# Performance work log

Measured on AMD Instinct MI355X. Metric: run time of the kernel, lower is better.

The kernel has to match this reference:

```python
import jax, jax.numpy as jnp
import numpy as np

N = 50000
E = 800000
G = 8
IN, HID, OUT = 128, 256, 128
BN_EPS = 1e-5


def _linear_params(key, fan_in, fan_out):
    k1, k2 = jax.random.split(key)
    s = 1.0 / np.sqrt(fan_in)
    w = jax.random.uniform(k1, (fan_out, fan_in), jnp.float32, -s, s)
    b = jax.random.uniform(k2, (fan_out,), jnp.float32, -s, s)
    return w, b


def setup_inputs() -> dict:
    key = jax.random.key(0)
    ks = jax.random.split(key, 16)
    inp = {
        "x": jax.random.normal(ks[0], (N, IN), jnp.float32),
        "src": jax.random.randint(ks[1], (E,), 0, N, jnp.int32),
        "dst": jax.random.randint(ks[2], (E,), 0, N, jnp.int32),
        "graph_ids": jnp.sort(jax.random.randint(ks[3], (N,), 0, G, jnp.int32)),
    }
    dims = [(IN, HID, HID), (HID, HID, HID), (HID, OUT, OUT)]
    for i, (d_in, d_mid, d_out) in enumerate(dims):
        kk = jax.random.split(ks[4 + i], 2)
        w1, b1 = _linear_params(kk[0], d_in, d_mid)
        w2, b2 = _linear_params(kk[1], d_mid, d_out)
        inp[f"w1_{i}"] = w1
        inp[f"b1_{i}"] = b1
        inp[f"w2_{i}"] = w2
        inp[f"b2_{i}"] = b2
        inp[f"eps_{i}"] = jnp.zeros((), jnp.float32)          # learn_eps, init 0
        inp[f"gamma_{i}"] = jnp.ones((d_out,), jnp.float32)   # BatchNorm weight
        inp[f"beta_{i}"] = jnp.zeros((d_out,), jnp.float32)   # BatchNorm bias
    return inp


def _gin_layer(h, src, dst, w1, b1, w2, b2, eps, gamma, beta):
    # GINConv: (1 + eps) * h_v + sum_{u in N(v)} h_u   (copy_u / sum)
    agg = jax.ops.segment_sum(h[src], dst, num_segments=N)
    z = (1.0 + eps) * h + agg
    # 2-layer MLP with ReLU
    z = jnp.maximum(z @ w1.T + b1, 0.0) @ w2.T + b2
    # BatchNorm1d (training-mode batch statistics, biased variance)
    mu = jnp.mean(z, axis=0)
    var = jnp.var(z, axis=0)
    return (z - mu) * jax.lax.rsqrt(var + BN_EPS) * gamma + beta


def reference(x, src, dst, graph_ids,
              w1_0, b1_0, w2_0, b2_0, eps_0, gamma_0, beta_0,
              w1_1, b1_1, w2_1, b2_1, eps_1, gamma_1, beta_1,
              w1_2, b1_2, w2_2, b2_2, eps_2, gamma_2, beta_2):
    h = _gin_layer(x, src, dst, w1_0, b1_0, w2_0, b2_0, eps_0, gamma_0, beta_0)
    h = jnp.maximum(h, 0.0)  # relu (dropout = identity in eval)
    h = _gin_layer(h, src, dst, w1_1, b1_1, w2_1, b2_1, eps_1, gamma_1, beta_1)
    h = jnp.maximum(h, 0.0)
    h = _gin_layer(h, src, dst, w1_2, b1_2, w2_2, b2_2, eps_2, gamma_2, beta_2)
    # dgl.mean_nodes: per-graph mean over nodes -> [G, OUT]
    sums = jax.ops.segment_sum(h, graph_ids, num_segments=G)
    counts = jax.ops.segment_sum(jnp.ones((N,), h.dtype), graph_ids, num_segments=G)
    return sums / jnp.maximum(counts, 1.0)[:, None]
```

## Files before the change

### kernel.cpp

```cpp
#include <hip/hip_runtime.h>

#define NG 8

typedef _Float16 half8  __attribute__((ext_vector_type(8)));
typedef float    f32x16 __attribute__((ext_vector_type(16)));


__global__ __launch_bounds__(256)
void k_cast16(const float* __restrict__ in, _Float16* __restrict__ out, int n8) {
    int i = blockIdx.x * 256 + threadIdx.x;
    if (i < n8) {
        const float4 a = *(const float4*)(in + (size_t)i * 8);
        const float4 b = *(const float4*)(in + (size_t)i * 8 + 4);
        half8 o;
        o[0] = (_Float16)a.x; o[1] = (_Float16)a.y; o[2] = (_Float16)a.z; o[3] = (_Float16)a.w;
        o[4] = (_Float16)b.x; o[5] = (_Float16)b.y; o[6] = (_Float16)b.z; o[7] = (_Float16)b.w;
        *(half8*)(out + (size_t)i * 8) = o;
    }
}

__global__ __launch_bounds__(256)
void k_castw(const float* __restrict__ w0, const float* __restrict__ w1,
             const float* __restrict__ w2, const float* __restrict__ w3,
             const float* __restrict__ w4, const float* __restrict__ w5,
             _Float16* __restrict__ o0, _Float16* __restrict__ o1,
             _Float16* __restrict__ o2, _Float16* __restrict__ o3,
             _Float16* __restrict__ o4, _Float16* __restrict__ o5) {
    int i = blockIdx.x * 256 + threadIdx.x;
    const float* in; _Float16* out; int off, lgC, K;
    if      (i <  4096) { in = w0; out = o0; off = 0;     lgC = 8; K = 128; }
    else if (i < 12288) { in = w1; out = o1; off = 4096;  lgC = 8; K = 256; }
    else if (i < 20480) { in = w2; out = o2; off = 12288; lgC = 8; K = 256; }
    else if (i < 28672) { in = w3; out = o3; off = 20480; lgC = 8; K = 256; }
    else if (i < 32768) { in = w4; out = o4; off = 28672; lgC = 7; K = 256; }
    else if (i < 34816) { in = w5; out = o5; off = 32768; lgC = 7; K = 128; }
    else return;
    int j = i - off;
    int kslot = j >> lgC;
    int c = j & ((1 << lgC) - 1);
    const float* s = in + (size_t)c * K + kslot * 8;
    const float4 a = *(const float4*)(s);
    const float4 b = *(const float4*)(s + 4);
    half8 o;
    o[0] = (_Float16)a.x; o[1] = (_Float16)a.y; o[2] = (_Float16)a.z; o[3] = (_Float16)a.w;
    o[4] = (_Float16)b.x; o[5] = (_Float16)b.y; o[6] = (_Float16)b.z; o[7] = (_Float16)b.w;
    *(half8*)(out + (size_t)j * 8) = o;
}


__global__ __launch_bounds__(256)
void k_deg(const int* __restrict__ dst, int* __restrict__ deg, int E) {
    int i = blockIdx.x * 256 + threadIdx.x;
    if (i < E) atomicAdd(&deg[dst[i]], 1);
}

__global__ __launch_bounds__(1024)
void k_scan_a(const int* __restrict__ deg, int* __restrict__ incl,
              int* __restrict__ bsum, int n) {
    __shared__ int s[1024];
    int t = threadIdx.x;
    int base = blockIdx.x * 1024;
    int v = (base + t < n) ? deg[base + t] : 0;
    s[t] = v;
    __syncthreads();
    for (int off = 1; off < 1024; off <<= 1) {
        int x = 0;
        if (t >= off) x = s[t - off];
        __syncthreads();
        if (t >= off) s[t] += x;
        __syncthreads();
    }
    if (base + t < n) incl[base + t] = s[t];
    if (t == 1023) bsum[blockIdx.x] = s[1023];
}

__global__ void k_scan_b(int* bsum, int nb) {
    if (threadIdx.x == 0 && blockIdx.x == 0) {
        int run = 0;
        for (int i = 0; i < nb; ++i) { int v = bsum[i]; bsum[i] = run; run += v; }
    }
}

__global__ __launch_bounds__(256)
void k_scan_c(const int* __restrict__ incl, const int* __restrict__ deg,
              const int* __restrict__ bsum, int* __restrict__ rowp, int n) {
    int i = blockIdx.x * 256 + threadIdx.x;
    if (i < n) rowp[i] = incl[i] - deg[i] + bsum[i >> 10];
}

__global__ __launch_bounds__(256)
void k_scatter(const int* __restrict__ src, const int* __restrict__ dst,
               const int* __restrict__ rowp, int* __restrict__ cur,
               int* __restrict__ ss, int E) {
    int i = blockIdx.x * 256 + threadIdx.x;
    if (i < E) {
        int d = dst[i];
        int pos = rowp[d] + atomicAdd(&cur[d], 1);
        ss[pos] = src[i];
    }
}


template<int K, bool AFFINE>
__global__ __launch_bounds__(256)
void k_agg16(const _Float16* __restrict__ h, const int* __restrict__ rowp,
             const int* __restrict__ deg, const int* __restrict__ ss,
             const float* __restrict__ eps, const float* __restrict__ scp,
             const float* __restrict__ shp, _Float16* __restrict__ z, int n) {
    constexpr int TPN = K / 8;
    constexpr int NPB = 256 / TPN;
    int node = blockIdx.x * NPB + threadIdx.x / TPN;
    int lane = threadIdx.x % TPN;
    if (node >= n) return;
    float e1 = 1.0f + eps[0];
    const int c0 = lane * 8;
    float sc[8], sh[8];
    if (AFFINE) {
#pragma unroll
        for (int e = 0; e < 8; ++e) { sc[e] = scp[c0 + e]; sh[e] = shp[c0 + e]; }
    }
    size_t base = (size_t)node * K + c0;
    half8 v = *(const half8*)(h + base);
    float a[8];
#pragma unroll
    for (int e = 0; e < 8; ++e) {
        float f = (float)v[e];
        if (AFFINE) f = fmaxf(f * sc[e] + sh[e], 0.0f);
        a[e] = f * e1;
    }
    int s  = rowp[node];
    int dn = deg[node];
    int j = 0;
    for (; j + 4 <= dn; j += 4) {
        int u0 = ss[s + j], u1 = ss[s + j + 1], u2 = ss[s + j + 2], u3 = ss[s + j + 3];
        half8 h0 = *(const half8*)(h + (size_t)u0 * K + c0);
        half8 h1 = *(const half8*)(h + (size_t)u1 * K + c0);
        half8 h2 = *(const half8*)(h + (size_t)u2 * K + c0);
        half8 h3 = *(const half8*)(h + (size_t)u3 * K + c0);
#pragma unroll
        for (int e = 0; e < 8; ++e) {
            float f0 = (float)h0[e], f1 = (float)h1[e];
            float f2 = (float)h2[e], f3 = (float)h3[e];
            if (AFFINE) {
                f0 = fmaxf(f0 * sc[e] + sh[e], 0.0f);
                f1 = fmaxf(f1 * sc[e] + sh[e], 0.0f);
                f2 = fmaxf(f2 * sc[e] + sh[e], 0.0f);
                f3 = fmaxf(f3 * sc[e] + sh[e], 0.0f);
            }
            a[e] += (f0 + f1) + (f2 + f3);
        }
    }
    for (; j < dn; ++j) {
        int u = ss[s + j];
        half8 hv = *(const half8*)(h + (size_t)u * K + c0);
#pragma unroll
        for (int e = 0; e < 8; ++e) {
            float f = (float)hv[e];
            if (AFFINE) f = fmaxf(f * sc[e] + sh[e], 0.0f);
            a[e] += f;
        }
    }
    half8 o;
#pragma unroll
    for (int e = 0; e < 8; ++e) o[e] = (_Float16)a[e];
    *(half8*)(z + base) = o;
}


template<int K, int MID, int MOUT>
__global__ __launch_bounds__(512)
void k_mlp3(const _Float16* __restrict__ A, const _Float16* __restrict__ W1,
            const float* __restrict__ b1, const _Float16* __restrict__ W2,
            const float* __restrict__ b2, _Float16* __restrict__ C,
            float* __restrict__ partial, int n, int ntiles) {
    constexpr int NK1 = K / 16;
    constexpr int NK2 = MID / 16;
    constexpr int MF1 = (MID == 256) ? 2 : 1;
    constexpr int MF2 = (MOUT == 256) ? 2 : 1;
    constexpr int NLD = K / 64;
    __shared__ char As[64 * 512];
    __shared__ char Ys[64 * 512];
    const int tid  = threadIdx.x;
    const int lane = tid & 63;
    const int wid  = tid >> 6;
    const int lo   = lane & 31;
    const int hi   = lane >> 5;

    const int wc1 = (MID == 256) ? wid : (wid & 3);
    const int wr1 = (MID == 256) ? 0   : (wid >> 2);
    const int colbase1 = wc1 * 32;
    const int wc2 = (MOUT == 256) ? wid : (wid & 3);
    const int wr2 = (MOUT == 256) ? 0   : (wid >> 2);
    const int colbase2 = wc2 * 32;

    half8 w1f[NK1], w2f[NK2];
#pragma unroll
    for (int ks = 0; ks < NK1; ++ks)
        w1f[ks] = *(const half8*)(W1 + ((size_t)(ks * 2 + hi) * MID + colbase1 + lo) * 8);
#pragma unroll
    for (int ks = 0; ks < NK2; ++ks)
        w2f[ks] = *(const half8*)(W2 + ((size_t)(ks * 2 + hi) * MOUT + colbase2 + lo) * 8);
    const float bb1 = b1[colbase1 + lo];
    const float bb2 = b2[colbase2 + lo];

    const int sr = tid >> 3;
    const int sl = tid & 7;
    const int g  = lane & 3;
    const int rl = lane >> 2;
    char* tb = Ys + wid * 2304;

    float s[8], q[8];
#pragma unroll
    for (int e = 0; e < 8; ++e) { s[e] = 0.f; q[e] = 0.f; }

    int tile = blockIdx.x;
    uint4 ar[NLD];
    if (tile < ntiles) {
        int ga = tile * 64 + sr; if (ga > n - 1) ga = n - 1;
        const char* Ab = (const char*)(A + (size_t)ga * K);
#pragma unroll
        for (int i = 0; i < NLD; ++i) ar[i] = *(const uint4*)(Ab + (sl + i * 8) * 16);
    }

    for (; tile < ntiles; tile += gridDim.x) {
        const int brow = tile * 64;

#pragma unroll
        for (int i = 0; i < NLD; ++i)
            *(uint4*)(As + sr * 512 + (((sl + i * 8) ^ (sr & 31)) << 4)) = ar[i];
        int nt = tile + gridDim.x;
        if (nt < ntiles) {
            int ga = nt * 64 + sr; if (ga > n - 1) ga = n - 1;
            const char* Ab = (const char*)(A + (size_t)ga * K);
#pragma unroll
            for (int i = 0; i < NLD; ++i) ar[i] = *(const uint4*)(Ab + (sl + i * 8) * 16);
        }
        __syncthreads();

        f32x16 acc1[MF1];
#pragma unroll
        for (int mf = 0; mf < MF1; ++mf)
#pragma unroll
            for (int e = 0; e < 16; ++e) acc1[mf][e] = 0.0f;
#pragma unroll
        for (int ks = 0; ks < NK1; ++ks) {
#pragma unroll
            for (int mf = 0; mf < MF1; ++mf) {
                int r = ((wr1 + mf) << 5) + lo;
                half8 af = *(const half8*)(As + r * 512 + ((ks * 32 + hi * 16) ^ ((r & 31) << 4)));
                acc1[mf] = __builtin_amdgcn_mfma_f32_32x32x16_f16(af, w1f[ks], acc1[mf], 0, 0, 0);
            }
        }
#pragma unroll
        for (int mf = 0; mf < MF1; ++mf) {
            int rb = ((wr1 + mf) << 5) + (hi << 2);
#pragma unroll
            for (int j = 0; j < 16; ++j) {
                int r = rb + (j & 3) + ((j >> 2) << 3);
                float v = fmaxf(acc1[mf][j] + bb1, 0.0f);
                *(_Float16*)(Ys + r * 512 + (((colbase1 + lo) * 2) ^ ((r & 31) << 4))) = (_Float16)v;
            }
        }
        __syncthreads();

        f32x16 acc2[MF2];
#pragma unroll
        for (int mf = 0; mf < MF2; ++mf)
#pragma unroll
            for (int e = 0; e < 16; ++e) acc2[mf][e] = 0.0f;
#pragma unroll
        for (int ks = 0; ks < NK2; ++ks) {
#pragma unroll
            for (int mf = 0; mf < MF2; ++mf) {
                int r = ((wr2 + mf) << 5) + lo;
                half8 af = *(const half8*)(Ys + r * 512 + ((ks * 32 + hi * 16) ^ ((r & 31) << 4)));
                acc2[mf] = __builtin_amdgcn_mfma_f32_32x32x16_f16(af, w2f[ks], acc2[mf], 0, 0, 0);
            }
        }
        __syncthreads();

#pragma unroll
        for (int mf = 0; mf < MF2; ++mf) {
#pragma unroll
            for (int j = 0; j < 16; ++j) {
                int tr = (j & 3) + ((j >> 2) << 3) + (hi << 2);
                *(_Float16*)(tb + tr * 72 + lo * 2) = (_Float16)(acc2[mf][j] + bb2);
            }
#pragma unroll
            for (int it = 0; it < 2; ++it) {
                int lr = it * 16 + rl;
                int grow = brow + ((wr2 + mf) << 5) + lr;
                half8 v = *(const half8*)(tb + lr * 72 + g * 16);
                if (grow < n) {
                    *(half8*)(C + (size_t)grow * MOUT + colbase2 + g * 8) = v;
#pragma unroll
                    for (int e = 0; e < 8; ++e) { float f = (float)v[e]; s[e] += f; q[e] += f * f; }
                }
            }
        }
    }

#pragma unroll
    for (int e = 0; e < 8; ++e) {
        for (int mk = 4; mk < 64; mk <<= 1) {
            s[e] += __shfl_xor(s[e], mk, 64);
            q[e] += __shfl_xor(q[e], mk, 64);
        }
    }
    if (lane < 4) {
        float* p = partial + ((size_t)blockIdx.x * 2 + wr2) * (2 * MOUT);
#pragma unroll
        for (int e = 0; e < 8; ++e) {
            p[colbase2 + lane * 8 + e]        = s[e];
            p[MOUT + colbase2 + lane * 8 + e] = q[e];
        }
    }
}


template<int M>
__global__ __launch_bounds__(256)
void k_bnred(const float* __restrict__ partial, const float* __restrict__ gamma,
             const float* __restrict__ beta, float* __restrict__ scale,
             float* __restrict__ shift, int n, int count, int step) {
    const int w = threadIdx.x >> 6, lane = threadIdx.x & 63;
    const int c = blockIdx.x * 4 + w;
    float s = 0.f, q = 0.f;
    for (int b = lane; b < count; b += 64) {
        const float* p = partial + (size_t)(b * step) * (2 * M);
        s += p[c];
        q += p[M + c];
    }
#pragma unroll
    for (int mk = 1; mk < 64; mk <<= 1) {
        s += __shfl_xor(s, mk, 64);
        q += __shfl_xor(q, mk, 64);
    }
    if (lane == 0) {
        float invN = 1.0f / (float)n;
        float mean = s * invN;
        float var  = q * invN - mean * mean;
        float sc   = rsqrtf(var + 1e-5f) * gamma[c];
        scale[c] = sc;
        shift[c] = beta[c] - mean * sc;
    }
}


__global__ __launch_bounds__(256)
void k_readout2(const _Float16* __restrict__ z, const float* __restrict__ scale,
                const float* __restrict__ shift, const int* __restrict__ gid,
                float* __restrict__ rpart, int* __restrict__ rcnt, int n) {
    __shared__ float ls[NG * 128];
    __shared__ int   lc[NG];
    for (int i = threadIdx.x; i < NG * 128; i += 256) ls[i] = 0.0f;
    if (threadIdx.x < NG) lc[threadIdx.x] = 0;
    __syncthreads();
    const int c16 = threadIdx.x & 15;
    const int ro  = threadIdx.x >> 4;
    const int c0  = c16 * 8;
    float sc[8], sh[8];
#pragma unroll
    for (int e = 0; e < 8; ++e) { sc[e] = scale[c0 + e]; sh[e] = shift[c0 + e]; }
    for (int r = blockIdx.x * 16 + ro; r < n; r += gridDim.x * 16) {
        int g = gid[r];
        half8 v = *(const half8*)(z + (size_t)r * 128 + c0);
#pragma unroll
        for (int e = 0; e < 8; ++e)
            atomicAdd(&ls[g * 128 + c0 + e], (float)v[e] * sc[e] + sh[e]);
        if (c16 == 0) atomicAdd(&lc[g], 1);
    }
    __syncthreads();
    float* p = rpart + (size_t)blockIdx.x * (NG * 128);
    for (int i = threadIdx.x; i < NG * 128; i += 256) p[i] = ls[i];
    if (threadIdx.x < NG) rcnt[blockIdx.x * NG + threadIdx.x] = lc[threadIdx.x];
}


__global__ __launch_bounds__(256)
void k_final3(const float* __restrict__ rpart, const int* __restrict__ rcnt,
              float* __restrict__ out, int nbr) {
    const int w = threadIdx.x >> 6, lane = threadIdx.x & 63;
    const int i = blockIdx.x * 4 + w;
    const int g = i >> 7;
    float s = 0.0f;
    int cnt = 0;
    for (int b = lane; b < nbr; b += 64) {
        s   += rpart[(size_t)b * (NG * 128) + i];
        cnt += rcnt[b * NG + g];
    }
#pragma unroll
    for (int mk = 1; mk < 64; mk <<= 1) {
        s   += __shfl_xor(s, mk, 64);
        cnt += __shfl_xor(cnt, mk, 64);
    }
    if (lane == 0) out[i] = s / fmaxf((float)cnt, 1.0f);
}


extern "C" void kernel_launch(void* const* d_in, const int* in_sizes, int n_in,
                              void* d_out, int out_size, void* d_ws, size_t ws_size,
                              hipStream_t stream) {
    const float* x   = (const float*)d_in[0];
    const int*   src = (const int*)d_in[1];
    const int*   dst = (const int*)d_in[2];
    const int*   gid = (const int*)d_in[3];
    const int n = in_sizes[0] / 128;
    const int E = in_sizes[1];

    auto align = [](size_t o) { return (o + 255) & ~(size_t)255; };
    char* ws = (char*)d_ws;
    size_t off = 0;
    const size_t SZ_H = align((size_t)n * 256 * sizeof(_Float16));
    const size_t SZ_I = align((size_t)n * sizeof(int));
    const int gx = (n + 63) / 64;
    const int NBLK = 512;
    const int RB   = 1024;

    _Float16* h0 = (_Float16*)(ws + off); off += align((size_t)n * 128 * sizeof(_Float16));
    _Float16* P0 = (_Float16*)(ws + off); off += SZ_H;
    _Float16* P1 = (_Float16*)(ws + off); off += SZ_H;
    int*   deg  = (int*)(ws + off);   off += SZ_I;
    int*   incl = (int*)(ws + off);   off += SZ_I;
    int*   rowp = (int*)(ws + off);   off += SZ_I;
    int*   cur  = (int*)(ws + off);   off += SZ_I;
    int*   bsum = (int*)(ws + off);   off += 256 * sizeof(int);
    int*   ss   = (int*)(ws + off);   off += align((size_t)E * sizeof(int));
    float* partial = (float*)(ws + off); off += align((size_t)(2 * NBLK) * 2 * 256 * sizeof(float));
    float* scale   = (float*)(ws + off); off += align(256 * sizeof(float));
    float* shiftb  = (float*)(ws + off); off += align(256 * sizeof(float));
    float* rpart = (float*)(ws + off); off += align((size_t)RB * NG * 128 * sizeof(float));
    int*   rcnt  = (int*)(ws + off);  off += align((size_t)RB * NG * sizeof(int));
    _Float16* wh[6];
    for (int i = 0; i < 6; ++i) { wh[i] = (_Float16*)(ws + off); off += align(65536 * sizeof(_Float16)); }

    k_cast16<<<(n * 128 / 8 + 255) / 256, 256, 0, stream>>>(x, h0, n * 128 / 8);
    k_castw<<<136, 256, 0, stream>>>(
        (const float*)d_in[4], (const float*)d_in[6],
        (const float*)d_in[11], (const float*)d_in[13],
        (const float*)d_in[18], (const float*)d_in[20],
        wh[0], wh[1], wh[2], wh[3], wh[4], wh[5]);

    hipMemsetAsync(deg, 0, (size_t)n * sizeof(int), stream);
    k_deg<<<(E + 255) / 256, 256, 0, stream>>>(dst, deg, E);
    int nb = (n + 1023) / 1024;
    k_scan_a<<<nb, 1024, 0, stream>>>(deg, incl, bsum, n);
    k_scan_b<<<1, 1, 0, stream>>>(bsum, nb);
    k_scan_c<<<(n + 255) / 256, 256, 0, stream>>>(incl, deg, bsum, rowp, n);
    hipMemsetAsync(cur, 0, (size_t)n * sizeof(int), stream);
    k_scatter<<<(E + 255) / 256, 256, 0, stream>>>(src, dst, rowp, cur, ss, E);

    for (int L = 0; L < 3; ++L) {
        const int base = 4 + 7 * L;
        const float* b1    = (const float*)d_in[base + 1];
        const float* b2    = (const float*)d_in[base + 3];
        const float* eps   = (const float*)d_in[base + 4];
        const float* gamma = (const float*)d_in[base + 5];
        const float* beta  = (const float*)d_in[base + 6];

        if (L == 0) {
            k_agg16<128, false><<<(n + 15) / 16, 256, 0, stream>>>(
                h0, rowp, deg, ss, eps, nullptr, nullptr, P1, n);
            k_mlp3<128, 256, 256><<<NBLK, 512, 0, stream>>>(P1, wh[0], b1, wh[1], b2, P0, partial, n, gx);
            k_bnred<256><<<64, 256, 0, stream>>>(partial, gamma, beta, scale, shiftb, n, NBLK, 2);
        } else if (L == 1) {
            k_agg16<256, true><<<(n + 7) / 8, 256, 0, stream>>>(
                P0, rowp, deg, ss, eps, scale, shiftb, P1, n);
            k_mlp3<256, 256, 256><<<NBLK, 512, 0, stream>>>(P1, wh[2], b1, wh[3], b2, P0, partial, n, gx);
            k_bnred<256><<<64, 256, 0, stream>>>(partial, gamma, beta, scale, shiftb, n, NBLK, 2);
        } else {
            k_agg16<256, true><<<(n + 7) / 8, 256, 0, stream>>>(
                P0, rowp, deg, ss, eps, scale, shiftb, P1, n);
            k_mlp3<256, 128, 128><<<NBLK, 512, 0, stream>>>(P1, wh[4], b1, wh[5], b2, P0, partial, n, gx);
            k_bnred<128><<<32, 256, 0, stream>>>(partial, gamma, beta, scale, shiftb, n, 2 * NBLK, 1);
        }
    }

    k_readout2<<<RB, 256, 0, stream>>>(P0, scale, shiftb, gid, rpart, rcnt, n);
    k_final3<<<256, 256, 0, stream>>>(rpart, rcnt, (float*)d_out, RB);
}
```

Before: 416.3 us.

## Merge setup kernels, drop rowp pass, give MLP epilogue own LDS, halve MLP grid

Fuses the x cast, weight cast and the deg/cur zeroing into one launch, which removes two memsets and a kernel. It also drops the k_scan_c pass by computing row offsets inline from incl, deg and bsum in the scatter and aggregation kernels. The MLP kernel gets a separate shared buffer for the per-wave transpose, so a __syncthreads can be removed, at the cost of about 18 KB more LDS per block. The MLP grid is halved to 256 blocks, which cuts partial-stat traffic but may lower parallelism.

```diff
diff --git a/kernel.cpp b/kernel.cpp
--- a/kernel.cpp
+++ b/kernel.cpp
@@ -7,44 +7,51 @@
 
 
 __global__ __launch_bounds__(256)
-void k_cast16(const float* __restrict__ in, _Float16* __restrict__ out, int n8) {
+void k_castall(const float* __restrict__ x, _Float16* __restrict__ h0,
+               const float* __restrict__ w0, const float* __restrict__ w1,
+               const float* __restrict__ w2, const float* __restrict__ w3,
+               const float* __restrict__ w4, const float* __restrict__ w5,
+               _Float16* __restrict__ o0, _Float16* __restrict__ o1,
+               _Float16* __restrict__ o2, _Float16* __restrict__ o3,
+               _Float16* __restrict__ o4, _Float16* __restrict__ o5,
+               int* __restrict__ deg, int* __restrict__ cur, int n) {
+    const int A  = n * 16;
+    const int B  = A + 34816;
+    const int ZD = (n + 3) / 4;
     int i = blockIdx.x * 256 + threadIdx.x;
-    if (i < n8) {
-        const float4 a = *(const float4*)(in + (size_t)i * 8);
-        const float4 b = *(const float4*)(in + (size_t)i * 8 + 4);
+    if (i < A) {
+        const float4 a = *(const float4*)(x + (size_t)i * 8);
+        const float4 b = *(const float4*)(x + (size_t)i * 8 + 4);
         half8 o;
         o[0] = (_Float16)a.x; o[1] = (_Float16)a.y; o[2] = (_Float16)a.z; o[3] = (_Float16)a.w;
         o[4] = (_Float16)b.x; o[5] = (_Float16)b.y; o[6] = (_Float16)b.z; o[7] = (_Float16)b.w;
-        *(half8*)(out + (size_t)i * 8) = o;
-    }
-}
-
-__global__ __launch_bounds__(256)
-void k_castw(const float* __restrict__ w0, const float* __restrict__ w1,
-             const float* __restrict__ w2, const float* __restrict__ w3,
-             const float* __restrict__ w4, const float* __restrict__ w5,
-             _Float16* __restrict__ o0, _Float16* __restrict__ o1,
-             _Float16* __restrict__ o2, _Float16* __restrict__ o3,
-             _Float16* __restrict__ o4, _Float16* __restrict__ o5) {
-    int i = blockIdx.x * 256 + threadIdx.x;
-    const float* in; _Float16* out; int off, lgC, K;
-    if      (i <  4096) { in = w0; out = o0; off = 0;     lgC = 8; K = 128; }
-    else if (i < 12288) { in = w1; out = o1; off = 4096;  lgC = 8; K = 256; }
-    else if (i < 20480) { in = w2; out = o2; off = 12288; lgC = 8; K = 256; }
-    else if (i < 28672) { in = w3; out = o3; off = 20480; lgC = 8; K = 256; }
-    else if (i < 32768) { in = w4; out = o4; off = 28672; lgC = 7; K = 256; }
-    else if (i < 34816) { in = w5; out = o5; off = 32768; lgC = 7; K = 128; }
-    else return;
-    int j = i - off;
-    int kslot = j >> lgC;
-    int c = j & ((1 << lgC) - 1);
-    const float* s = in + (size_t)c * K + kslot * 8;
-    const float4 a = *(const float4*)(s);
-    const float4 b = *(const float4*)(s + 4);
-    half8 o;
-    o[0] = (_Float16)a.x; o[1] = (_Float16)a.y; o[2] = (_Float16)a.z; o[3] = (_Float16)a.w;
-    o[4] = (_Float16)b.x; o[5] = (_Float16)b.y; o[6] = (_Float16)b.z; o[7] = (_Float16)b.w;
-    *(half8*)(out + (size_t)j * 8) = o;
+        *(half8*)(h0 + (size_t)i * 8) = o;
+    } else if (i < B) {
+        int i2 = i - A;
+        const float* in; _Float16* out; int off, lgC, K;
+        if      (i2 <  4096) { in = w0; out = o0; off = 0;     lgC = 8; K = 128; }
+        else if (i2 < 12288) { in = w1; out = o1; off = 4096;  lgC = 8; K = 256; }
+        else if (i2 < 20480) { in = w2; out = o2; off = 12288; lgC = 8; K = 256; }
+        else if (i2 < 28672) { in = w3; out = o3; off = 20480; lgC = 8; K = 256; }
+        else if (i2 < 32768) { in = w4; out = o4; off = 28672; lgC = 7; K = 256; }
+        else                 { in = w5; out = o5; off = 32768; lgC = 7; K = 128; }
+        int j = i2 - off;
+        int kslot = j >> lgC;
+        int c = j & ((1 << lgC) - 1);
+        const float* s = in + (size_t)c * K + kslot * 8;
+        const float4 a = *(const float4*)(s);
+        const float4 b = *(const float4*)(s + 4);
+        half8 o;
+        o[0] = (_Float16)a.x; o[1] = (_Float16)a.y; o[2] = (_Float16)a.z; o[3] = (_Float16)a.w;
+        o[4] = (_Float16)b.x; o[5] = (_Float16)b.y; o[6] = (_Float16)b.z; o[7] = (_Float16)b.w;
+        *(half8*)(out + (size_t)j * 8) = o;
+    } else if (i < B + ZD) {
+        int j = i - B;
+        *(int4*)(deg + j * 4) = (int4){0, 0, 0, 0};
+    } else if (i < B + 2 * ZD) {
+        int j = i - B - ZD;
+        *(int4*)(cur + j * 4) = (int4){0, 0, 0, 0};
+    }
 }
 
 
@@ -82,20 +89,15 @@
 }
 
 __global__ __launch_bounds__(256)
-void k_scan_c(const int* __restrict__ incl, const int* __restrict__ deg,
-              const int* __restrict__ bsum, int* __restrict__ rowp, int n) {
-    int i = blockIdx.x * 256 + threadIdx.x;
-    if (i < n) rowp[i] = incl[i] - deg[i] + bsum[i >> 10];
-}
-
-__global__ __launch_bounds__(256)
 void k_scatter(const int* __restrict__ src, const int* __restrict__ dst,
-               const int* __restrict__ rowp, int* __restrict__ cur,
+               const int* __restrict__ incl, const int* __restrict__ deg,
+               const int* __restrict__ bsum, int* __restrict__ cur,
                int* __restrict__ ss, int E) {
     int i = blockIdx.x * 256 + threadIdx.x;
     if (i < E) {
         int d = dst[i];
-        int pos = rowp[d] + atomicAdd(&cur[d], 1);
+        int base = incl[d] - deg[d] + bsum[d >> 10];
+        int pos = base + atomicAdd(&cur[d], 1);
         ss[pos] = src[i];
     }
 }
@@ -103,10 +105,11 @@
 
 template<int K, bool AFFINE>
 __global__ __launch_bounds__(256)
-void k_agg16(const _Float16* __restrict__ h, const int* __restrict__ rowp,
-             const int* __restrict__ deg, const int* __restrict__ ss,
-             const float* __restrict__ eps, const float* __restrict__ scp,
-             const float* __restrict__ shp, _Float16* __restrict__ z, int n) {
+void k_agg16(const _Float16* __restrict__ h, const int* __restrict__ incl,
+             const int* __restrict__ deg, const int* __restrict__ bsum,
+             const int* __restrict__ ss, const float* __restrict__ eps,
+             const float* __restrict__ scp, const float* __restrict__ shp,
+             _Float16* __restrict__ z, int n) {
     constexpr int TPN = K / 8;
     constexpr int NPB = 256 / TPN;
     int node = blockIdx.x * NPB + threadIdx.x / TPN;
@@ -128,8 +131,8 @@
         if (AFFINE) f = fmaxf(f * sc[e] + sh[e], 0.0f);
         a[e] = f * e1;
     }
-    int s  = rowp[node];
     int dn = deg[node];
+    int s  = incl[node] - dn + bsum[node >> 10];
     int j = 0;
     for (; j + 4 <= dn; j += 4) {
         int u0 = ss[s + j], u1 = ss[s + j + 1], u2 = ss[s + j + 2], u3 = ss[s + j + 3];
@@ -180,6 +183,7 @@
     constexpr int NLD = K / 64;
     __shared__ char As[64 * 512];
     __shared__ char Ys[64 * 512];
+    __shared__ char tbs[8 * 2304];
     const int tid  = threadIdx.x;
     const int lane = tid & 63;
     const int wid  = tid >> 6;
@@ -207,7 +211,7 @@
     const int sl = tid & 7;
     const int g  = lane & 3;
     const int rl = lane >> 2;
-    char* tb = Ys + wid * 2304;
+    char* tb = tbs + wid * 2304;
 
     float s[8], q[8];
 #pragma unroll
@@ -277,7 +281,6 @@
                 acc2[mf] = __builtin_amdgcn_mfma_f32_32x32x16_f16(af, w2f[ks], acc2[mf], 0, 0, 0);
             }
         }
-        __syncthreads();
 
 #pragma unroll
         for (int mf = 0; mf < MF2; ++mf) {
@@ -414,7 +417,7 @@
     const size_t SZ_H = align((size_t)n * 256 * sizeof(_Float16));
     const size_t SZ_I = align((size_t)n * sizeof(int));
     const int gx = (n + 63) / 64;
-    const int NBLK = 512;
+    const int NBLK = 256;
     const int RB   = 1024;
 
     _Float16* h0 = (_Float16*)(ws + off); off += align((size_t)n * 128 * sizeof(_Float16));
@@ -422,7 +425,6 @@
     _Float16* P1 = (_Float16*)(ws + off); off += SZ_H;
     int*   deg  = (int*)(ws + off);   off += SZ_I;
     int*   incl = (int*)(ws + off);   off += SZ_I;
-    int*   rowp = (int*)(ws + off);   off += SZ_I;
     int*   cur  = (int*)(ws + off);   off += SZ_I;
     int*   bsum = (int*)(ws + off);   off += 256 * sizeof(int);
     int*   ss   = (int*)(ws + off);   off += align((size_t)E * sizeof(int));
@@ -434,21 +436,24 @@
     _Float16* wh[6];
     for (int i = 0; i < 6; ++i) { wh[i] = (_Float16*)(ws + off); off += align(65536 * sizeof(_Float16)); }
 
-    k_cast16<<<(n * 128 / 8 + 255) / 256, 256, 0, stream>>>(x, h0, n * 128 / 8);
-    k_castw<<<136, 256, 0, stream>>>(
-        (const float*)d_in[4], (const float*)d_in[6],
-        (const float*)d_in[11], (const float*)d_in[13],
-        (const float*)d_in[18], (const float*)d_in[20],
-        wh[0], wh[1], wh[2], wh[3], wh[4], wh[5]);
-
-    hipMemsetAsync(deg, 0, (size_t)n * sizeof(int), stream);
+    {
+        int A = n * 16;
+        int ZD = (n + 3) / 4;
+        int total = A + 34816 + 2 * ZD;
+        k_castall<<<(total + 255) / 256, 256, 0, stream>>>(
+            x, h0,
+            (const float*)d_in[4], (const float*)d_in[6],
+            (const float*)d_in[11], (const float*)d_in[13],
+            (const float*)d_in[18], (const float*)d_in[20],
+            wh[0], wh[1], wh[2], wh[3], wh[4], wh[5],
+            deg, cur, n);
+    }
+
     k_deg<<<(E + 255) / 256, 256, 0, stream>>>(dst, deg, E);
     int nb = (n + 1023) / 1024;
     k_scan_a<<<nb, 1024, 0, stream>>>(deg, incl, bsum, n);
     k_scan_b<<<1, 1, 0, stream>>>(bsum, nb);
-    k_scan_c<<<(n + 255) / 256, 256, 0, stream>>>(incl, deg, bsum, rowp, n);
-    hipMemsetAsync(cur, 0, (size_t)n * sizeof(int), stream);
-    k_scatter<<<(E + 255) / 256, 256, 0, stream>>>(src, dst, rowp, cur, ss, E);
+    k_scatter<<<(E + 255) / 256, 256, 0, stream>>>(src, dst, incl, deg, bsum, cur, ss, E);
 
     for (int L = 0; L < 3; ++L) {
         const int base = 4 + 7 * L;
@@ -460,17 +465,17 @@
 
         if (L == 0) {
             k_agg16<128, false><<<(n + 15) / 16, 256, 0, stream>>>(
-                h0, rowp, deg, ss, eps, nullptr, nullptr, P1, n);
+                h0, incl, deg, bsum, ss, eps, nullptr, nullptr, P1, n);
             k_mlp3<128, 256, 256><<<NBLK, 512, 0, stream>>>(P1, wh[0], b1, wh[1], b2, P0, partial, n, gx);
             k_bnred<256><<<64, 256, 0, stream>>>(partial, gamma, beta, scale, shiftb, n, NBLK, 2);
         } else if (L == 1) {
             k_agg16<256, true><<<(n + 7) / 8, 256, 0, stream>>>(
-                P0, rowp, deg, ss, eps, scale, shiftb, P1, n);
+                P0, incl, deg, bsum, ss, eps, scale, shiftb, P1, n);
             k_mlp3<256, 256, 256><<<NBLK, 512, 0, stream>>>(P1, wh[2], b1, wh[3], b2, P0, partial, n, gx);
             k_bnred<256><<<64, 256, 0, stream>>>(partial, gamma, beta, scale, shiftb, n, NBLK, 2);
         } else {
             k_agg16<256, true><<<(n + 7) / 8, 256, 0, stream>>>(
-                P0, rowp, deg, ss, eps, scale, shiftb, P1, n);
+                P0, incl, deg, bsum, ss, eps, scale, shiftb, P1, n);
             k_mlp3<256, 128, 128><<<NBLK, 512, 0, stream>>>(P1, wh[4], b1, wh[5], b2, P0, partial, n, gx);
             k_bnred<128><<<32, 256, 0, stream>>>(partial, gamma, beta, scale, shiftb, n, 2 * NBLK, 1);
         }
```

Measured after the change: 405.1 us. -2.7%, faster.
